# Kernel optimization log

Hardware: AMD Instinct MI355X
Metric: run time of the kernel (lower is better)

## Reference

```python
import jax, jax.numpy as jnp
import numpy as np

HIDDEN = 4096
NUM_BLOCKS = 8
BLOCK = HIDDEN // NUM_BLOCKS  # 512


def setup_inputs() -> dict:
    key = jax.random.key(0)
    k1, k2, k3, k4 = jax.random.split(key, 4)
    return {
        "weight": jax.random.normal(k1, (HIDDEN, HIDDEN), dtype=jnp.float32) * 0.02,
        "bias": jax.random.normal(k2, (HIDDEN,), dtype=jnp.float32) * 0.02,
        "x": jax.random.normal(k3, (4, 2048, HIDDEN), dtype=jnp.float32),
        "proj_R": jax.random.normal(k4, (NUM_BLOCKS, BLOCK, BLOCK), dtype=jnp.float32) * 0.02,
        "layer_idx": 0,
    }


def _cayley_batch(A):
    # Q = (I - S) @ inv(I + S + 1e-6*I), S = 0.5*(A - A^T), batched over blocks
    r = A.shape[-1]
    I = jnp.eye(r, dtype=A.dtype)
    S = 0.5 * (A - jnp.swapaxes(A, -2, -1))
    Minv = jnp.linalg.inv(I + S + 1e-6 * I)
    return jnp.einsum('bij,bjk->bik', I - S, Minv)


def reference(weight, bias, x, proj_R, layer_idx):
    Q = _cayley_batch(proj_R)                     # [nb, bs, bs], orthogonal blocks
    nb, bs, _ = Q.shape
    # block_diag(Q) @ weight == batched block-row matmul (off-diagonal blocks are zero)
    Wb = weight.reshape(nb, bs, weight.shape[1])  # [nb, bs, in]
    filt = jnp.einsum('bij,bjk->bik', Q, Wb).reshape(nb * bs, weight.shape[1])
    # F.linear(x, filt, bias)
    return jnp.einsum('bsi,oi->bso', x, filt) + bias
```

## Files before the change

### kernel.cpp

```cpp
#include <hip/hip_runtime.h>

typedef unsigned short u16;
typedef __attribute__((ext_vector_type(8))) short bf16x8;
typedef __attribute__((ext_vector_type(4))) float f32x4;
typedef __attribute__((ext_vector_type(8))) unsigned short u16x8;
typedef __attribute__((ext_vector_type(4))) unsigned short u16x4;

__device__ __forceinline__ u16 f2bf(float f){
  unsigned int u = __builtin_bit_cast(unsigned int, f);
  u += 0x7FFFu + ((u >> 16) & 1u);
  return (u16)(u >> 16);
}
__device__ __forceinline__ float bf2f(u16 h){
  unsigned int u = ((unsigned int)h) << 16;
  return __builtin_bit_cast(float, u);
}

__device__ __forceinline__ void load16(const u16* g, u16* s){
  __builtin_amdgcn_global_load_lds((const __attribute__((address_space(1))) unsigned int*)g,
                                   (__attribute__((address_space(3))) unsigned int*)s,
                                   16, 0, 0);
}

__global__ __launch_bounds__(256) void prep_sw(const float* __restrict__ R, const float* __restrict__ W,
                                               u16* __restrict__ Sbf, u16* __restrict__ Dbf,
                                               u16* __restrict__ Wt){
  const int blk = blockIdx.x;
  const int t = threadIdx.x;
  if (blk < 8192){
    int idx = blk * 256 + t;
    int b = idx >> 18;
    int i = (idx >> 9) & 511;
    int j = idx & 511;
    float a  = R[idx];
    float at = R[(b << 18) + (j << 9) + i];
    float s = 0.5f * (a - at);
    Sbf[idx] = f2bf(s);
    Dbf[idx] = f2bf((i == j ? 2.000003f : 0.0f) - 2.000001f * s);
  }
  __shared__ float tile[32][33];
  const int fx = blk & 127, fy = (blk >> 7) & 15, fz = blk >> 11;
  const int i0 = fx << 5, j0 = fy << 5;
  const int r = t >> 3, c = (t & 7) << 2;
  float4 v = *(const float4*)&W[(size_t)((fz << 9) + j0 + r) * 4096 + i0 + c];
  tile[r][c+0] = v.x; tile[r][c+1] = v.y; tile[r][c+2] = v.z; tile[r][c+3] = v.w;
  __syncthreads();
  u16x4 o = { f2bf(tile[c+0][r]), f2bf(tile[c+1][r]), f2bf(tile[c+2][r]), f2bf(tile[c+3][r]) };
  *(u16x4*)&Wt[((size_t)fz << 21) + (size_t)(i0 + r) * 512 + j0 + c] = o;
}

__global__ __launch_bounds__(256) void conv_bf16(const float* __restrict__ src, u16* __restrict__ dst){
  size_t i = (size_t)blockIdx.x * 256 + threadIdx.x;
  const float4* s = (const float4*)src + i * 2;
  float4 v0 = s[0], v1 = s[1];
  u16x8 o = { f2bf(v0.x), f2bf(v0.y), f2bf(v0.z), f2bf(v0.w),
              f2bf(v1.x), f2bf(v1.y), f2bf(v1.z), f2bf(v1.w) };
  *(u16x8*)(dst + i * 8) = o;
}

template<int EPI>
__global__ __launch_bounds__(256) void gemm_ns(const u16* __restrict__ A, const u16* __restrict__ B,
                                               void* __restrict__ Cout, void* __restrict__ aux,
                                               void* __restrict__ aux2,
                                               int M, int N, int K){
  const int bz = blockIdx.z;
  const char* Ab = (const char*)(A + (size_t)bz * M * K);
  const char* Bb = (const char*)(B + (size_t)bz * N * K);
  const int m0 = blockIdx.y << 6, n0 = blockIdx.x << 6;
  __shared__ __align__(16) char As[4096];
  __shared__ __align__(16) char Bs[4096];
  const int t = threadIdx.x;
  const int w = t >> 6, l = t & 63;
  const int wm = w >> 1, wn = w & 1;
  const size_t Kb = (size_t)K << 1;
  const int sR = t >> 2;
  const int sK = ((t ^ (t >> 2)) & 3) << 4;
  const int kq = (((l >> 4) ^ l) & 3) << 4;
  const int aRd = ((wm << 5) + (l & 15)) * 64 + kq;
  const int bRd = ((wn << 5) + (l & 15)) * 64 + kq;
  f32x4 acc[2][2] = {};
  for (int k0 = 0; k0 < K; k0 += 32){
    const size_t kb = (size_t)k0 << 1;
    load16((const u16*)(Ab + (size_t)(m0 + sR) * Kb + kb + sK), (u16*)(As + t * 16));
    load16((const u16*)(Bb + (size_t)(n0 + sR) * Kb + kb + sK), (u16*)(Bs + t * 16));
    __syncthreads();
    bf16x8 aF[2], bF[2];
#pragma unroll
    for (int mf = 0; mf < 2; ++mf) aF[mf] = *(const bf16x8*)(As + aRd + (mf << 10));
#pragma unroll
    for (int nf = 0; nf < 2; ++nf) bF[nf] = *(const bf16x8*)(Bs + bRd + (nf << 10));
#pragma unroll
    for (int mf = 0; mf < 2; ++mf)
#pragma unroll
      for (int nf = 0; nf < 2; ++nf)
        acc[mf][nf] = __builtin_amdgcn_mfma_f32_16x16x32_bf16(aF[mf], bF[nf], acc[mf][nf], 0, 0, 0);
    __syncthreads();
  }
#pragma unroll
  for (int mf = 0; mf < 2; ++mf){
#pragma unroll
    for (int nf = 0; nf < 2; ++nf){
      const int col = n0 + (wn << 5) + (nf << 4) + (l & 15);
#pragma unroll
      for (int q = 0; q < 4; ++q){
        const int row = m0 + (wm << 5) + (mf << 4) + ((l >> 4) << 2) + q;
        float v = acc[mf][nf][q];
        size_t gi = ((size_t)bz * M + row) * N + col;
        size_t g2 = (((size_t)bz * M + row) << 10) + col;
        if (EPI == 2){
          ((u16*)Cout)[gi] = f2bf(v);
        } else if (EPI == 3){
          ((u16*)Cout)[gi] = f2bf((row == col ? 2.0f : 0.0f) - v);
        } else if (EPI == 9){
          ((u16*)Cout)[gi] = f2bf(v - (row == col ? 1.0f : 0.0f));
        } else {
          float p = v + (row == col ? 1.000002f : 0.0f);
          u16 ph = f2bf(p);
          ((u16*)Cout)[g2] = ph;
          ((u16*)Cout)[g2 + 512] = f2bf(p - bf2f(ph));
          const float beta = 0.8264463f;
          u16 x1 = f2bf((row == col ? 2.0f * beta : 0.0f) - beta * beta * p);
          ((u16*)aux)[gi] = x1;
          ((u16*)aux2)[g2] = x1;
          ((u16*)aux2)[g2 + 512] = x1;
        }
      }
    }
  }
}

template<int EPI>
__global__ __launch_bounds__(512, 2) void gemm256(const u16* __restrict__ A, const u16* __restrict__ B,
                                                  void* __restrict__ Cout, const float* __restrict__ aux,
                                                  int M, int N, int K){
  __shared__ __align__(16) char lds[131072];
  const int bz = blockIdx.z;
  const char* Ab = (const char*)(A + (size_t)bz * M * K);
  const char* Bb = (const char*)(B + (size_t)bz * N * K);
  const int NB = N >> 8;
  const int nwg = gridDim.x;
  const int bid = blockIdx.x;
  const int swzb = (bid & 7) * (nwg >> 3) + (bid >> 3);
  const int m0 = (swzb / NB) << 8;
  const int n0 = (swzb % NB) << 8;
  const int tid = threadIdx.x;
  const int w = tid >> 6, l = tid & 63;
  const int wm = w >> 2, wn = w & 3;
  const size_t Kb = (size_t)K << 1;
  const int NT = K >> 6;
  const int sRow = tid >> 3;
  const int sCol = ((tid & 7) << 4) ^ ((sRow & 7) << 4);
  const int sDst = tid << 4;
  const char* aS = Ab + (size_t)(m0 + sRow) * Kb + sCol;
  const char* bS = Bb + (size_t)(n0 + sRow) * Kb + sCol;
  const int lrow = (l & 15) << 7;
  const int kq0 = (((l >> 4) << 4)) ^ ((l & 7) << 4);
  const int aOff = (wm << 14) + lrow;
  const int bOff = 32768 + ((wn >> 1) << 14) + ((wn & 1) << 13) + lrow;

#define STAGE_H(isB, h, tt) { \
    const int _lo = (((tt) & 1) << 16) + ((isB) << 15) + ((h) << 14); \
    const char* _s = ((isB) ? bS : aS) + ((size_t)((h) << 7)) * Kb + ((size_t)(tt) << 7); \
    load16((const u16*)_s, (u16*)(lds + _lo + sDst)); \
    load16((const u16*)(_s + (Kb << 6)), (u16*)(lds + _lo + 8192 + sDst)); }

#define RD_A(bufb, UQ) \
  _Pragma("unroll") for (int i2 = 0; i2 < 4; ++i2){ \
    aF[i2][0] = *(const bf16x8*)(lds + (bufb) + aOff + ((UQ) << 13) + (i2 << 11) + kq0); \
    aF[i2][1] = *(const bf16x8*)(lds + (bufb) + aOff + ((UQ) << 13) + (i2 << 11) + (kq0 ^ 64)); }

#define RD_B(bufb, VQ) \
  _Pragma("unroll") for (int j2 = 0; j2 < 2; ++j2){ \
    bF[VQ][j2][0] = *(const bf16x8*)(lds + (bufb) + bOff + ((VQ) << 12) + (j2 << 11) + kq0); \
    bF[VQ][j2][1] = *(const bf16x8*)(lds + (bufb) + bOff + ((VQ) << 12) + (j2 << 11) + (kq0 ^ 64)); }

#define MFMA16(UQ, VQ) \
    _Pragma("unroll") for (int i2 = 0; i2 < 4; ++i2) \
      _Pragma("unroll") for (int j2 = 0; j2 < 2; ++j2){ \
        acc[(UQ)*4+i2][(VQ)*2+j2] = __builtin_amdgcn_mfma_f32_16x16x32_bf16(aF[i2][0], bF[VQ][j2][0], acc[(UQ)*4+i2][(VQ)*2+j2], 0, 0, 0); \
        acc[(UQ)*4+i2][(VQ)*2+j2] = __builtin_amdgcn_mfma_f32_16x16x32_bf16(aF[i2][1], bF[VQ][j2][1], acc[(UQ)*4+i2][(VQ)*2+j2], 0, 0, 0); }

#define BAR asm volatile("s_barrier" ::: "memory");
#define VM0 asm volatile("s_waitcnt vmcnt(0)" ::: "memory");

  bf16x8 aF[4][2], bF[2][2][2];
  f32x4 acc[8][4] = {};

  STAGE_H(0,0,0) STAGE_H(1,0,0) STAGE_H(0,1,0) STAGE_H(1,1,0)
  VM0 BAR

#define KTILE(t, bufb) { \
    RD_A(bufb, 0) RD_B(bufb, 0) \
    if ((t) + 1 < NT) { STAGE_H(0,0,(t)+1) STAGE_H(1,0,(t)+1) } \
    MFMA16(0,0) \
    RD_B(bufb, 1) \
    if ((t) + 1 < NT) { STAGE_H(0,1,(t)+1) STAGE_H(1,1,(t)+1) } \
    MFMA16(0,1) \
    RD_A(bufb, 1) \
    MFMA16(1,1) \
    MFMA16(1,0) \
    __builtin_amdgcn_sched_barrier(0); \
    VM0 BAR }

#pragma unroll 1
  for (int tp = 0; tp < NT; tp += 2){
    KTILE(tp, 0)
    KTILE(tp+1, 65536)
  }
#undef KTILE

#pragma unroll
  for (int mf = 0; mf < 8; ++mf){
#pragma unroll
    for (int nf = 0; nf < 4; ++nf){
      const int col = n0 + (wn << 6) + (nf << 4) + (l & 15);
#pragma unroll
      for (int q = 0; q < 4; ++q){
        const int row = m0 + (wm << 7) + (mf << 4) + ((l >> 4) << 2) + q;
        float v = acc[mf][nf][q];
        if (EPI == 0){
          ((float*)Cout)[(size_t)row * N + col] = v + aux[col];
        } else {
          ((u16*)Cout)[((size_t)bz * M + row) * N + col] = f2bf(v);
        }
      }
    }
  }
#undef STAGE_H
#undef RD_A
#undef RD_B
#undef MFMA16
#undef BAR
#undef VM0
}

extern "C" void kernel_launch(void* const* d_in, const int* in_sizes, int n_in,
                              void* d_out, int out_size, void* d_ws, size_t ws_size,
                              hipStream_t stream){
  const float* W    = (const float*)d_in[0];
  const float* bias = (const float*)d_in[1];
  const float* x    = (const float*)d_in[2];
  const float* R    = (const float*)d_in[3];
  (void)in_sizes; (void)n_in; (void)out_size; (void)ws_size;

  char* ws = (char*)d_ws;
  const size_t MiB = (size_t)1 << 20;
  u16*   Sbf  = (u16*)(ws + 0 * MiB);
  u16*   Dbf  = (u16*)(ws + 4 * MiB);
  u16*   X1   = (u16*)(ws + 8 * MiB);
  u16*   Ybf  = (u16*)(ws + 12 * MiB);
  u16*   X2   = (u16*)(ws + 16 * MiB);
  u16*   Phl  = (u16*)(ws + 20 * MiB);
  u16*   X1d  = (u16*)(ws + 28 * MiB);
  u16*   G    = Sbf;
  u16*   filt = (u16*)(ws + 4 * MiB);
  u16*   Wt   = (u16*)(ws + 64 * MiB);
  u16*   xbf  = (u16*)(ws + 36 * MiB);

  const dim3 gNS(8, 8, 8);

  prep_sw<<<16384, 256, 0, stream>>>(R, W, Sbf, Dbf, Wt);
  gemm_ns<11><<<gNS, 256, 0, stream>>>(Sbf, Sbf, Phl, X1, X1d, 512, 512, 512);
  gemm_ns<3><<<gNS, 256, 0, stream>>>(Phl, X1d, Ybf, nullptr, nullptr, 512, 512, 1024);
  gemm_ns<2><<<gNS, 256, 0, stream>>>(X1, Ybf, X2, nullptr, nullptr, 512, 512, 512);
  gemm_ns<9><<<gNS, 256, 0, stream>>>(Dbf, X2, G, nullptr, nullptr, 512, 512, 512);
  gemm256<2><<<dim3(32, 1, 8), 512, 0, stream>>>(G, Wt, (void*)filt, nullptr, 512, 4096, 512);
  conv_bf16<<<16384, 256, 0, stream>>>(x, xbf);
  gemm256<0><<<dim3(512, 1, 1), 512, 0, stream>>>(xbf, filt, d_out, bias, 8192, 4096, 4096);
}
```

Measured before the change: 346.1 us.

## Use 1024-thread workgroups with 64x64 per-wave tiles in gemm256

Doubles the gemm256 workgroup from 512 to 1024 threads (16 waves in a 4x4 grid), each wave owning a 64x64 output sub-tile instead of 128x64. Staging is simplified so each thread issues two loads per operand per K-tile, and the interleaved MFMA/LDS-read schedule is replaced by a simpler read-all-then-compute pattern over two K halves. This cuts accumulator registers per wave and raises wave count per workgroup, but gives up the 2-workgroup-per-CU launch bound and the finer-grained overlap of loads with MFMAs. Each wave now does more LDS reads per MFMA.

```diff
diff --git a/kernel.cpp b/kernel.cpp
--- a/kernel.cpp
+++ b/kernel.cpp
@@ -130,9 +130,9 @@
 }
 
 template<int EPI>
-__global__ __launch_bounds__(512, 2) void gemm256(const u16* __restrict__ A, const u16* __restrict__ B,
-                                                  void* __restrict__ Cout, const float* __restrict__ aux,
-                                                  int M, int N, int K){
+__global__ __launch_bounds__(1024) void gemm256(const u16* __restrict__ A, const u16* __restrict__ B,
+                                                void* __restrict__ Cout, const float* __restrict__ aux,
+                                                int M, int N, int K){
   __shared__ __align__(16) char lds[131072];
   const int bz = blockIdx.z;
   const char* Ab = (const char*)(A + (size_t)bz * M * K);
@@ -153,52 +153,42 @@
   const int sDst = tid << 4;
   const char* aS = Ab + (size_t)(m0 + sRow) * Kb + sCol;
   const char* bS = Bb + (size_t)(n0 + sRow) * Kb + sCol;
-  const int lrow = (l & 15) << 7;
   const int kq0 = (((l >> 4) << 4)) ^ ((l & 7) << 4);
-  const int aOff = (wm << 14) + lrow;
-  const int bOff = 32768 + ((wn >> 1) << 14) + ((wn & 1) << 13) + lrow;
-
-#define STAGE_H(isB, h, tt) { \
-    const int _lo = (((tt) & 1) << 16) + ((isB) << 15) + ((h) << 14); \
-    const char* _s = ((isB) ? bS : aS) + ((size_t)((h) << 7)) * Kb + ((size_t)(tt) << 7); \
+  const int aOff = ((wm << 6) + (l & 15)) << 7;
+  const int bOff = 32768 + (((wn << 6) + (l & 15)) << 7);
+
+#define STAGE_X(isB, tt) { \
+    const int _lo = (((tt) & 1) << 16) + ((isB) << 15); \
+    const char* _s = ((isB) ? bS : aS) + ((size_t)(tt) << 7); \
     load16((const u16*)_s, (u16*)(lds + _lo + sDst)); \
-    load16((const u16*)(_s + (Kb << 6)), (u16*)(lds + _lo + 8192 + sDst)); }
-
-#define RD_A(bufb, UQ) \
-  _Pragma("unroll") for (int i2 = 0; i2 < 4; ++i2){ \
-    aF[i2][0] = *(const bf16x8*)(lds + (bufb) + aOff + ((UQ) << 13) + (i2 << 11) + kq0); \
-    aF[i2][1] = *(const bf16x8*)(lds + (bufb) + aOff + ((UQ) << 13) + (i2 << 11) + (kq0 ^ 64)); }
-
-#define RD_B(bufb, VQ) \
-  _Pragma("unroll") for (int j2 = 0; j2 < 2; ++j2){ \
-    bF[VQ][j2][0] = *(const bf16x8*)(lds + (bufb) + bOff + ((VQ) << 12) + (j2 << 11) + kq0); \
-    bF[VQ][j2][1] = *(const bf16x8*)(lds + (bufb) + bOff + ((VQ) << 12) + (j2 << 11) + (kq0 ^ 64)); }
-
-#define MFMA16(UQ, VQ) \
-    _Pragma("unroll") for (int i2 = 0; i2 < 4; ++i2) \
-      _Pragma("unroll") for (int j2 = 0; j2 < 2; ++j2){ \
-        acc[(UQ)*4+i2][(VQ)*2+j2] = __builtin_amdgcn_mfma_f32_16x16x32_bf16(aF[i2][0], bF[VQ][j2][0], acc[(UQ)*4+i2][(VQ)*2+j2], 0, 0, 0); \
-        acc[(UQ)*4+i2][(VQ)*2+j2] = __builtin_amdgcn_mfma_f32_16x16x32_bf16(aF[i2][1], bF[VQ][j2][1], acc[(UQ)*4+i2][(VQ)*2+j2], 0, 0, 0); }
+    load16((const u16*)(_s + (Kb << 7)), (u16*)(lds + _lo + 16384 + sDst)); }
+
+#define RD_A(bufb, kx) \
+  _Pragma("unroll") for (int mf = 0; mf < 4; ++mf) \
+    aF[mf] = *(const bf16x8*)(lds + (bufb) + aOff + (mf << 11) + (kq0 ^ (kx)));
+#define RD_B(bufb, kx) \
+  _Pragma("unroll") for (int nf = 0; nf < 4; ++nf) \
+    bF[nf] = *(const bf16x8*)(lds + (bufb) + bOff + (nf << 11) + (kq0 ^ (kx)));
+#define MFMA16 \
+  _Pragma("unroll") for (int mf = 0; mf < 4; ++mf) \
+    _Pragma("unroll") for (int nf = 0; nf < 4; ++nf) \
+      acc[mf][nf] = __builtin_amdgcn_mfma_f32_16x16x32_bf16(aF[mf], bF[nf], acc[mf][nf], 0, 0, 0);
 
 #define BAR asm volatile("s_barrier" ::: "memory");
 #define VM0 asm volatile("s_waitcnt vmcnt(0)" ::: "memory");
 
-  bf16x8 aF[4][2], bF[2][2][2];
-  f32x4 acc[8][4] = {};
-
-  STAGE_H(0,0,0) STAGE_H(1,0,0) STAGE_H(0,1,0) STAGE_H(1,1,0)
+  bf16x8 aF[4], bF[4];
+  f32x4 acc[4][4] = {};
+
+  STAGE_X(0, 0) STAGE_X(1, 0)
   VM0 BAR
 
 #define KTILE(t, bufb) { \
+    if ((t) + 1 < NT) { STAGE_X(0, (t)+1) STAGE_X(1, (t)+1) } \
     RD_A(bufb, 0) RD_B(bufb, 0) \
-    if ((t) + 1 < NT) { STAGE_H(0,0,(t)+1) STAGE_H(1,0,(t)+1) } \
-    MFMA16(0,0) \
-    RD_B(bufb, 1) \
-    if ((t) + 1 < NT) { STAGE_H(0,1,(t)+1) STAGE_H(1,1,(t)+1) } \
-    MFMA16(0,1) \
-    RD_A(bufb, 1) \
-    MFMA16(1,1) \
-    MFMA16(1,0) \
+    MFMA16 \
+    RD_A(bufb, 64) RD_B(bufb, 64) \
+    MFMA16 \
     __builtin_amdgcn_sched_barrier(0); \
     VM0 BAR }
 
@@ -208,15 +198,21 @@
     KTILE(tp+1, 65536)
   }
 #undef KTILE
-
-#pragma unroll
-  for (int mf = 0; mf < 8; ++mf){
+#undef STAGE_X
+#undef RD_A
+#undef RD_B
+#undef MFMA16
+#undef BAR
+#undef VM0
+
+#pragma unroll
+  for (int mf = 0; mf < 4; ++mf){
 #pragma unroll
     for (int nf = 0; nf < 4; ++nf){
       const int col = n0 + (wn << 6) + (nf << 4) + (l & 15);
 #pragma unroll
       for (int q = 0; q < 4; ++q){
-        const int row = m0 + (wm << 7) + (mf << 4) + ((l >> 4) << 2) + q;
+        const int row = m0 + (wm << 6) + (mf << 4) + ((l >> 4) << 2) + q;
         float v = acc[mf][nf][q];
         if (EPI == 0){
           ((float*)Cout)[(size_t)row * N + col] = v + aux[col];
@@ -226,12 +222,6 @@
       }
     }
   }
-#undef STAGE_H
-#undef RD_A
-#undef RD_B
-#undef MFMA16
-#undef BAR
-#undef VM0
 }
 
 extern "C" void kernel_launch(void* const* d_in, const int* in_sizes, int n_in,
@@ -264,7 +254,7 @@
   gemm_ns<3><<<gNS, 256, 0, stream>>>(Phl, X1d, Ybf, nullptr, nullptr, 512, 512, 1024);
   gemm_ns<2><<<gNS, 256, 0, stream>>>(X1, Ybf, X2, nullptr, nullptr, 512, 512, 512);
   gemm_ns<9><<<gNS, 256, 0, stream>>>(Dbf, X2, G, nullptr, nullptr, 512, 512, 512);
-  gemm256<2><<<dim3(32, 1, 8), 512, 0, stream>>>(G, Wt, (void*)filt, nullptr, 512, 4096, 512);
+  gemm256<2><<<dim3(32, 1, 8), 1024, 0, stream>>>(G, Wt, (void*)filt, nullptr, 512, 4096, 512);
   conv_bf16<<<16384, 256, 0, stream>>>(x, xbf);
-  gemm256<0><<<dim3(512, 1, 1), 512, 0, stream>>>(xbf, filt, d_out, bias, 8192, 4096, 4096);
-}
+  gemm256<0><<<dim3(512, 1, 1), 1024, 0, stream>>>(xbf, filt, d_out, bias, 8192, 4096, 4096);
+}
```

Measured after the change: 363.2 us. +4.9%, slower.

## Fuse prep and Newton-Schulz GEMM chain into one cooperative kernel with grid syncs

Applied to the files above, without the earlier changes.

Replaces the prep kernel and the four small 512x512 batched GEMM launches with a single cooperative kernel of 512 blocks, separating the stages with grid.sync(). Prep work is spread across the 512 blocks with strided loops. The goal is to cut launch gaps and tail effects between small dependent kernels. In exchange it adds grid-wide barrier costs and lowers parallelism for the prep phase, and the cooperative launch requires all 512 blocks to be resident at once.

```diff
diff --git a/kernel.cpp b/kernel.cpp
--- a/kernel.cpp
+++ b/kernel.cpp
@@ -1,4 +1,7 @@
 #include <hip/hip_runtime.h>
+#include <hip/hip_cooperative_groups.h>
+
+namespace cg = cooperative_groups;
 
 typedef unsigned short u16;
 typedef __attribute__((ext_vector_type(8))) short bf16x8;
@@ -20,33 +23,6 @@
   __builtin_amdgcn_global_load_lds((const __attribute__((address_space(1))) unsigned int*)g,
                                    (__attribute__((address_space(3))) unsigned int*)s,
                                    16, 0, 0);
-}
-
-__global__ __launch_bounds__(256) void prep_sw(const float* __restrict__ R, const float* __restrict__ W,
-                                               u16* __restrict__ Sbf, u16* __restrict__ Dbf,
-                                               u16* __restrict__ Wt){
-  const int blk = blockIdx.x;
-  const int t = threadIdx.x;
-  if (blk < 8192){
-    int idx = blk * 256 + t;
-    int b = idx >> 18;
-    int i = (idx >> 9) & 511;
-    int j = idx & 511;
-    float a  = R[idx];
-    float at = R[(b << 18) + (j << 9) + i];
-    float s = 0.5f * (a - at);
-    Sbf[idx] = f2bf(s);
-    Dbf[idx] = f2bf((i == j ? 2.000003f : 0.0f) - 2.000001f * s);
-  }
-  __shared__ float tile[32][33];
-  const int fx = blk & 127, fy = (blk >> 7) & 15, fz = blk >> 11;
-  const int i0 = fx << 5, j0 = fy << 5;
-  const int r = t >> 3, c = (t & 7) << 2;
-  float4 v = *(const float4*)&W[(size_t)((fz << 9) + j0 + r) * 4096 + i0 + c];
-  tile[r][c+0] = v.x; tile[r][c+1] = v.y; tile[r][c+2] = v.z; tile[r][c+3] = v.w;
-  __syncthreads();
-  u16x4 o = { f2bf(tile[c+0][r]), f2bf(tile[c+1][r]), f2bf(tile[c+2][r]), f2bf(tile[c+3][r]) };
-  *(u16x4*)&Wt[((size_t)fz << 21) + (size_t)(i0 + r) * 512 + j0 + c] = o;
 }
 
 __global__ __launch_bounds__(256) void conv_bf16(const float* __restrict__ src, u16* __restrict__ dst){
@@ -59,17 +35,15 @@
 }
 
 template<int EPI>
-__global__ __launch_bounds__(256) void gemm_ns(const u16* __restrict__ A, const u16* __restrict__ B,
-                                               void* __restrict__ Cout, void* __restrict__ aux,
-                                               void* __restrict__ aux2,
-                                               int M, int N, int K){
-  const int bz = blockIdx.z;
-  const char* Ab = (const char*)(A + (size_t)bz * M * K);
-  const char* Bb = (const char*)(B + (size_t)bz * N * K);
-  const int m0 = blockIdx.y << 6, n0 = blockIdx.x << 6;
-  __shared__ __align__(16) char As[4096];
-  __shared__ __align__(16) char Bs[4096];
-  const int t = threadIdx.x;
+__device__ __forceinline__ void ns_core(const u16* __restrict__ A, const u16* __restrict__ B,
+                                        void* __restrict__ Cout, void* __restrict__ aux,
+                                        void* __restrict__ aux2, int K,
+                                        int blk, int t, char* As, char* Bs){
+  const int bz = blk >> 6;
+  const int m0 = ((blk >> 3) & 7) << 6;
+  const int n0 = (blk & 7) << 6;
+  const char* Ab = (const char*)(A + (size_t)bz * 512 * K);
+  const char* Bb = (const char*)(B + (size_t)bz * 512 * K);
   const int w = t >> 6, l = t & 63;
   const int wm = w >> 1, wn = w & 1;
   const size_t Kb = (size_t)K << 1;
@@ -105,8 +79,8 @@
       for (int q = 0; q < 4; ++q){
         const int row = m0 + (wm << 5) + (mf << 4) + ((l >> 4) << 2) + q;
         float v = acc[mf][nf][q];
-        size_t gi = ((size_t)bz * M + row) * N + col;
-        size_t g2 = (((size_t)bz * M + row) << 10) + col;
+        size_t gi = ((size_t)bz * 512 + row) * 512 + col;
+        size_t g2 = (((size_t)bz * 512 + row) << 10) + col;
         if (EPI == 2){
           ((u16*)Cout)[gi] = f2bf(v);
         } else if (EPI == 3){
@@ -127,6 +101,54 @@
       }
     }
   }
+}
+
+__global__ __launch_bounds__(256) void ns_coop(const float* __restrict__ R, const float* __restrict__ W,
+                                               u16* __restrict__ Sbf, u16* __restrict__ Dbf,
+                                               u16* __restrict__ Wt, u16* __restrict__ Phl,
+                                               u16* __restrict__ X1, u16* __restrict__ X1d,
+                                               u16* __restrict__ Ybf, u16* __restrict__ X2,
+                                               u16* __restrict__ G){
+  cg::grid_group grid = cg::this_grid();
+  __shared__ __align__(16) char As[4096];
+  __shared__ __align__(16) char Bs[4096];
+  __shared__ float tileT[32][33];
+  const int blk = blockIdx.x;
+  const int t = threadIdx.x;
+
+#pragma unroll 1
+  for (int it = 0; it < 16; ++it){
+    int idx = (it * 512 + blk) * 256 + t;
+    int b = idx >> 18;
+    int i = (idx >> 9) & 511;
+    int j = idx & 511;
+    float a  = R[idx];
+    float at = R[(b << 18) + (j << 9) + i];
+    float s = 0.5f * (a - at);
+    Sbf[idx] = f2bf(s);
+    Dbf[idx] = f2bf((i == j ? 2.000003f : 0.0f) - 2.000001f * s);
+  }
+#pragma unroll 1
+  for (int it = 0; it < 32; ++it){
+    int flat = it * 512 + blk;
+    const int fx = flat & 127, fy = (flat >> 7) & 15, fz = flat >> 11;
+    const int i0 = fx << 5, j0 = fy << 5;
+    const int r = t >> 3, c = (t & 7) << 2;
+    float4 v = *(const float4*)&W[(size_t)((fz << 9) + j0 + r) * 4096 + i0 + c];
+    tileT[r][c+0] = v.x; tileT[r][c+1] = v.y; tileT[r][c+2] = v.z; tileT[r][c+3] = v.w;
+    __syncthreads();
+    u16x4 o = { f2bf(tileT[c+0][r]), f2bf(tileT[c+1][r]), f2bf(tileT[c+2][r]), f2bf(tileT[c+3][r]) };
+    *(u16x4*)&Wt[((size_t)fz << 21) + (size_t)(i0 + r) * 512 + j0 + c] = o;
+    __syncthreads();
+  }
+  grid.sync();
+  ns_core<11>(Sbf, Sbf, Phl, X1, X1d, 512, blk, t, As, Bs);
+  grid.sync();
+  ns_core<3>(Phl, X1d, Ybf, nullptr, nullptr, 1024, blk, t, As, Bs);
+  grid.sync();
+  ns_core<2>(X1, Ybf, X2, nullptr, nullptr, 512, blk, t, As, Bs);
+  grid.sync();
+  ns_core<9>(Dbf, X2, G, nullptr, nullptr, 512, blk, t, As, Bs);
 }
 
 template<int EPI>
@@ -257,13 +279,10 @@
   u16*   Wt   = (u16*)(ws + 64 * MiB);
   u16*   xbf  = (u16*)(ws + 36 * MiB);
 
-  const dim3 gNS(8, 8, 8);
-
-  prep_sw<<<16384, 256, 0, stream>>>(R, W, Sbf, Dbf, Wt);
-  gemm_ns<11><<<gNS, 256, 0, stream>>>(Sbf, Sbf, Phl, X1, X1d, 512, 512, 512);
-  gemm_ns<3><<<gNS, 256, 0, stream>>>(Phl, X1d, Ybf, nullptr, nullptr, 512, 512, 1024);
-  gemm_ns<2><<<gNS, 256, 0, stream>>>(X1, Ybf, X2, nullptr, nullptr, 512, 512, 512);
-  gemm_ns<9><<<gNS, 256, 0, stream>>>(Dbf, X2, G, nullptr, nullptr, 512, 512, 512);
+  void* args[] = { (void*)&R, (void*)&W, (void*)&Sbf, (void*)&Dbf, (void*)&Wt,
+                   (void*)&Phl, (void*)&X1, (void*)&X1d, (void*)&Ybf, (void*)&X2,
+                   (void*)&G };
+  hipLaunchCooperativeKernel((const void*)ns_coop, dim3(512), dim3(256), args, 0, stream);
   gemm256<2><<<dim3(32, 1, 8), 512, 0, stream>>>(G, Wt, (void*)filt, nullptr, 512, 4096, 512);
   conv_bf16<<<16384, 256, 0, stream>>>(x, xbf);
   gemm256<0><<<dim3(512, 1, 1), 512, 0, stream>>>(xbf, filt, d_out, bias, 8192, 4096, 4096);
```

Measured after the change: 610.8 us. 76.5% more time.
